# Kernel tuning notes

Measured on AMD Instinct MI355X. Metric: run time of the kernel, lower is better.

Reference implementation:

```python
import jax, jax.numpy as jnp
import numpy as np


def _causal_mask(n):
    # pixelSNAIL get_causal_mask: strict lower triangular (pixel i attends to pixels < i)
    return jnp.tril(jnp.ones((n, n), dtype=jnp.float32), k=-1)


def setup_inputs() -> dict:
    key = jax.random.key(0)
    kq, kk, kv = jax.random.split(key, 3)
    B, H, W, C, CM = 32, 32, 32, 128, 256
    return {
        "query": jax.random.normal(kq, (B, H, W, C), dtype=jnp.float32),
        "key": jax.random.normal(kk, (B, H, W, C), dtype=jnp.float32),
        "value": jax.random.normal(kv, (B, H, W, CM), dtype=jnp.float32),
    }


def reference(query, key, value):
    B = query.shape[0]
    C = key.shape[-1]
    CM = value.shape[-1]
    Nk = int(np.prod(key.shape[1:-1]))
    Nq = int(np.prod(query.shape[1:-1]))
    q = query.reshape(B, Nq, C)
    k = key.reshape(B, Nk, C)
    v = value.reshape(B, Nk, CM)
    # raw QK^T (no 1/sqrt(d) scaling in original)
    dot = jnp.einsum('bqc,bkc->bqk', q, k)
    # NON-STANDARD: softmax over full row first, then multiply by strict causal mask
    probs = jax.nn.softmax(dot, axis=-1) * _causal_mask(Nq)[None]
    mixed = jnp.einsum('bqk,bkm->bqm', probs, v)
    return mixed.reshape(query.shape[:-1] + (CM,))
```

## Files before the change

kernel.cpp:

```cpp
#include <hip/hip_runtime.h>


typedef __attribute__((ext_vector_type(8))) short short8;
typedef __attribute__((ext_vector_type(4))) float floatx4;

#define MFMA16(a, b, c) __builtin_amdgcn_mfma_f32_16x16x32_bf16((a), (b), (c), 0, 0, 0)

constexpr int N = 1024, C = 128, CM = 256, BATCH = 32;
constexpr int BM = 32;
constexpr int BN = 32;
constexpr int NT = N / BN;
constexpr int KFRAG = BN * C;
constexpr int VFRAG = BN * CM;
constexpr int PSTR = 40;

__device__ __forceinline__ unsigned short f2bf(float x) {
    unsigned int u = __float_as_uint(x);
    u += 0x7fffu + ((u >> 16) & 1u);
    return (unsigned short)(u >> 16);
}
__device__ __forceinline__ float bf2f(unsigned short h) {
    return __uint_as_float(((unsigned int)h) << 16);
}
__device__ __forceinline__ uint4 pack8(const unsigned short* s) {
    uint4 u;
    u.x = (unsigned)s[0] | ((unsigned)s[1] << 16);
    u.y = (unsigned)s[2] | ((unsigned)s[3] << 16);
    u.z = (unsigned)s[4] | ((unsigned)s[5] << 16);
    u.w = (unsigned)s[6] | ((unsigned)s[7] << 16);
    return u;
}
__device__ __forceinline__ void gl2lds16(const unsigned short* g, unsigned short* l) {
    __builtin_amdgcn_global_load_lds(
        (const __attribute__((address_space(1))) void*)g,
        (__attribute__((address_space(3))) void*)l, 16, 0, 0);
}

__global__ __launch_bounds__(256, 4)
void prep_kernel(const float* __restrict__ kg, const float* __restrict__ vg,
                 unsigned short* __restrict__ khi, unsigned short* __restrict__ klo,
                 unsigned short* __restrict__ vf)
{
    constexpr int KP = 132;
    constexpr int VP = 260;
    __shared__ __align__(16) float S[BN * VP];

    const int tid = threadIdx.x;
    const int tile = blockIdx.x, bat = blockIdx.y;
    const int n0 = tile * BN;
    const float* kb = kg + (size_t)bat * N * C;
    const float* vb = vg + (size_t)bat * N * CM;

#pragma unroll
    for (int i = 0; i < 4; ++i) {
        int f = tid + i * 256;
        int row = f >> 5, c4 = f & 31;
        float4 x = *(const float4*)(kb + (size_t)(n0 + row) * C + c4 * 4);
        *(float4*)(&S[row * KP + c4 * 4]) = x;
    }
    __syncthreads();
    {
        unsigned short* khb = khi + ((size_t)bat * NT + tile) * KFRAG;
        unsigned short* klb = klo + ((size_t)bat * NT + tile) * KFRAG;
#pragma unroll
        for (int i = 0; i < 2; ++i) {
            int ch = tid + i * 256;
            int r = ch & 15, qd = (ch >> 4) & 3, ks = (ch >> 6) & 3, t = ch >> 8;
            const float* src = &S[(t * 16 + r) * KP + ks * 32 + qd * 8];
            unsigned short hi[8], lo[8];
#pragma unroll
            for (int j = 0; j < 8; ++j) {
                float x = src[j];
                unsigned short h = f2bf(x);
                hi[j] = h;
                lo[j] = f2bf(x - bf2f(h));
            }
            *(uint4*)(khb + (size_t)ch * 8) = pack8(hi);
            *(uint4*)(klb + (size_t)ch * 8) = pack8(lo);
        }
    }
    __syncthreads();
#pragma unroll
    for (int i = 0; i < 8; ++i) {
        int f = tid + i * 256;
        int row = f >> 6, c4 = f & 63;
        float4 x = *(const float4*)(vb + (size_t)(n0 + row) * CM + c4 * 4);
        *(float4*)(&S[row * VP + c4 * 4]) = x;
    }
    __syncthreads();
    {
        unsigned short* vfb = vf + ((size_t)bat * NT + tile) * VFRAG;
#pragma unroll
        for (int i = 0; i < 4; ++i) {
            int ch = tid + i * 256;
            int r = ch & 15, qd = (ch >> 4) & 3, ct = ch >> 6;
            unsigned short o[8];
#pragma unroll
            for (int j = 0; j < 8; ++j)
                o[j] = f2bf(S[(qd * 8 + j) * VP + ct * 16 + r]);
            *(uint4*)(vfb + (size_t)ch * 8) = pack8(o);
        }
    }
}

__global__ __launch_bounds__(256, 4)
void attn_kernel(const float* __restrict__ qg, float* __restrict__ og,
                 const unsigned short* __restrict__ khi,
                 const unsigned short* __restrict__ klo,
                 const unsigned short* __restrict__ vf)
{
    __shared__ __align__(16) unsigned short sKhi[KFRAG];
    __shared__ __align__(16) unsigned short sKlo[KFRAG];
    __shared__ __align__(16) unsigned short sV[VFRAG];
    __shared__ __align__(16) unsigned short sP[4 * 16 * PSTR];

    const int tid = threadIdx.x;
    const int w = tid >> 6, ln = tid & 63;
    const int r = ln & 15, qd = ln >> 4;
    const int rowgrp = w >> 1;
    const int cmhalf = w & 1;
    const int bat = blockIdx.x;
    const int qt = blockIdx.y;
    const int q0 = qt * BM;

    const float* qb = qg + (size_t)bat * N * C;
    float* ob = og + (size_t)bat * N * CM;
    const unsigned short* khb = khi + (size_t)bat * NT * KFRAG;
    const unsigned short* klb = klo + (size_t)bat * NT * KFRAG;
    const unsigned short* vfb = vf + (size_t)bat * NT * VFRAG;

    short8 qhi[4], qlo[4];
    {
        const float* qr = qb + (size_t)(q0 + rowgrp * 16 + r) * C + qd * 8;
#pragma unroll
        for (int ks = 0; ks < 4; ++ks) {
            float4 a = *(const float4*)(qr + ks * 32);
            float4 b = *(const float4*)(qr + ks * 32 + 4);
            float xs[8] = {a.x, a.y, a.z, a.w, b.x, b.y, b.z, b.w};
            short8 h, l;
#pragma unroll
            for (int j = 0; j < 8; ++j) {
                unsigned short hb = f2bf(xs[j]);
                h[j] = (short)hb;
                l[j] = (short)f2bf(xs[j] - bf2f(hb));
            }
            qhi[ks] = h;
            qlo[ks] = l;
        }
    }

    floatx4 oacc[8];
#pragma unroll
    for (int ct = 0; ct < 8; ++ct) oacc[ct] = (floatx4){0.f, 0.f, 0.f, 0.f};
    float lsum[4] = {0.f, 0.f, 0.f, 0.f};
    const int irow = q0 + rowgrp * 16 + qd * 4;
    unsigned short* wP = &sP[w * 16 * PSTR];

    for (int tile = 0; tile < NT; ++tile) {
        const bool pv = (tile <= qt);

        {
            const unsigned short* sk = khb + (size_t)tile * KFRAG;
            gl2lds16(sk + (size_t)tid * 8,         &sKhi[tid * 8]);
            gl2lds16(sk + (size_t)(tid + 256) * 8, &sKhi[(tid + 256) * 8]);
            const unsigned short* sl = klb + (size_t)tile * KFRAG;
            gl2lds16(sl + (size_t)tid * 8,         &sKlo[tid * 8]);
            gl2lds16(sl + (size_t)(tid + 256) * 8, &sKlo[(tid + 256) * 8]);
            if (pv) {
                const unsigned short* sv = vfb + (size_t)tile * VFRAG;
#pragma unroll
                for (int i = 0; i < 4; ++i)
                    gl2lds16(sv + (size_t)(tid + i * 256) * 8, &sV[(tid + i * 256) * 8]);
            }
        }
        __syncthreads();

#pragma unroll
        for (int t = 0; t < 2; ++t) {
            floatx4 acc = (floatx4){0.f, 0.f, 0.f, 0.f};
#pragma unroll
            for (int ks = 0; ks < 4; ++ks) {
                short8 bh = *(const short8*)(&sKhi[(((t * 4 + ks) * 64) + ln) * 8]);
                short8 bl = *(const short8*)(&sKlo[(((t * 4 + ks) * 64) + ln) * 8]);
                acc = MFMA16(qhi[ks], bh, acc);
                acc = MFMA16(qlo[ks], bh, acc);
                acc = MFMA16(qhi[ks], bl, acc);
            }
            const int jglob = tile * BN + t * 16 + r;
#pragma unroll
            for (int rg = 0; rg < 4; ++rg) {
                float p = __expf(acc[rg] - 40.0f);
                lsum[rg] += p;
                if (pv) {
                    float pm = (jglob < irow + rg) ? p : 0.0f;
                    wP[(qd * 4 + rg) * PSTR + t * 16 + r] = f2bf(pm);
                }
            }
        }

        if (pv) {
            asm volatile("s_waitcnt lgkmcnt(0)" ::: "memory");
            short8 ap = *(const short8*)(&wP[r * PSTR + qd * 8]);
#pragma unroll
            for (int ct = 0; ct < 8; ++ct) {
                int ctg = cmhalf * 8 + ct;
                short8 bv = *(const short8*)(&sV[(ctg * 64 + ln) * 8]);
                oacc[ct] = MFMA16(ap, bv, oacc[ct]);
            }
        }
        __syncthreads();
    }

#pragma unroll
    for (int rg = 0; rg < 4; ++rg) {
        float v = lsum[rg];
        v += __shfl_xor(v, 1);
        v += __shfl_xor(v, 2);
        v += __shfl_xor(v, 4);
        v += __shfl_xor(v, 8);
        lsum[rg] = v;
    }

#pragma unroll
    for (int rg = 0; rg < 4; ++rg) {
        float inv = 1.0f / lsum[rg];
        float* orow = ob + (size_t)(q0 + rowgrp * 16 + qd * 4 + rg) * CM + cmhalf * 128;
#pragma unroll
        for (int ct = 0; ct < 8; ++ct)
            orow[ct * 16 + r] = oacc[ct][rg] * inv;
    }
}

extern "C" void kernel_launch(void* const* d_in, const int* in_sizes, int n_in,
                              void* d_out, int out_size, void* d_ws, size_t ws_size,
                              hipStream_t stream) {
    const float* q = (const float*)d_in[0];
    const float* k = (const float*)d_in[1];
    const float* v = (const float*)d_in[2];
    float* o = (float*)d_out;
    (void)n_in; (void)in_sizes; (void)out_size; (void)ws_size;

    unsigned short* khi = (unsigned short*)d_ws;
    unsigned short* klo = khi + (size_t)BATCH * NT * KFRAG;
    unsigned short* vf  = klo + (size_t)BATCH * NT * KFRAG;

    prep_kernel<<<dim3(NT, BATCH), dim3(256), 0, stream>>>(k, v, khi, klo, vf);
    attn_kernel<<<dim3(BATCH, N / BM), dim3(256), 0, stream>>>(q, o, khi, klo, vf);
}
```

Before: 175.0 us.

## Double-buffer K tiles, widen query tile to 64 rows, drop LDS staging in prep

The attention kernel now handles 64 query rows per block, with each wave owning 16 rows across all 256 value columns. This halves the number of times each K/V tile is streamed per batch. K hi/lo tiles are double-buffered, with the next tile prefetched through global_load_lds under explicit vmcnt waits and raw s_barrier, and the three split-bf16 MFMAs now use independent accumulators to break the dependency chain. The prep kernel drops its shared-memory staging and reads global memory directly, which gives strided uncoalesced V reads. The changes cost more accumulator registers (occupancy hint lowered to 2) and fewer blocks in the grid.

```diff
diff --git a/kernel.cpp b/kernel.cpp
--- a/kernel.cpp
+++ b/kernel.cpp
@@ -7,7 +7,7 @@
 #define MFMA16(a, b, c) __builtin_amdgcn_mfma_f32_16x16x32_bf16((a), (b), (c), 0, 0, 0)
 
 constexpr int N = 1024, C = 128, CM = 256, BATCH = 32;
-constexpr int BM = 32;
+constexpr int BM = 64;
 constexpr int BN = 32;
 constexpr int NT = N / BN;
 constexpr int KFRAG = BN * C;
@@ -36,89 +36,65 @@
         (__attribute__((address_space(3))) void*)l, 16, 0, 0);
 }
 
-__global__ __launch_bounds__(256, 4)
+__global__ __launch_bounds__(256, 8)
 void prep_kernel(const float* __restrict__ kg, const float* __restrict__ vg,
                  unsigned short* __restrict__ khi, unsigned short* __restrict__ klo,
                  unsigned short* __restrict__ vf)
 {
-    constexpr int KP = 132;
-    constexpr int VP = 260;
-    __shared__ __align__(16) float S[BN * VP];
-
     const int tid = threadIdx.x;
     const int tile = blockIdx.x, bat = blockIdx.y;
     const int n0 = tile * BN;
     const float* kb = kg + (size_t)bat * N * C;
     const float* vb = vg + (size_t)bat * N * CM;
-
+    unsigned short* khb = khi + ((size_t)bat * NT + tile) * KFRAG;
+    unsigned short* klb = klo + ((size_t)bat * NT + tile) * KFRAG;
+    unsigned short* vfb = vf + ((size_t)bat * NT + tile) * VFRAG;
+
+#pragma unroll
+    for (int i = 0; i < 2; ++i) {
+        int ch = tid + i * 256;
+        int r = ch & 15, qd = (ch >> 4) & 3, ks = (ch >> 6) & 3, t = ch >> 8;
+        const float* src = kb + (size_t)(n0 + t * 16 + r) * C + ks * 32 + qd * 8;
+        float4 a = *(const float4*)src;
+        float4 b = *(const float4*)(src + 4);
+        float xs[8] = {a.x, a.y, a.z, a.w, b.x, b.y, b.z, b.w};
+        unsigned short hi[8], lo[8];
+#pragma unroll
+        for (int j = 0; j < 8; ++j) {
+            unsigned short h = f2bf(xs[j]);
+            hi[j] = h;
+            lo[j] = f2bf(xs[j] - bf2f(h));
+        }
+        *(uint4*)(khb + (size_t)ch * 8) = pack8(hi);
+        *(uint4*)(klb + (size_t)ch * 8) = pack8(lo);
+    }
 #pragma unroll
     for (int i = 0; i < 4; ++i) {
-        int f = tid + i * 256;
-        int row = f >> 5, c4 = f & 31;
-        float4 x = *(const float4*)(kb + (size_t)(n0 + row) * C + c4 * 4);
-        *(float4*)(&S[row * KP + c4 * 4]) = x;
-    }
-    __syncthreads();
-    {
-        unsigned short* khb = khi + ((size_t)bat * NT + tile) * KFRAG;
-        unsigned short* klb = klo + ((size_t)bat * NT + tile) * KFRAG;
-#pragma unroll
-        for (int i = 0; i < 2; ++i) {
-            int ch = tid + i * 256;
-            int r = ch & 15, qd = (ch >> 4) & 3, ks = (ch >> 6) & 3, t = ch >> 8;
-            const float* src = &S[(t * 16 + r) * KP + ks * 32 + qd * 8];
-            unsigned short hi[8], lo[8];
-#pragma unroll
-            for (int j = 0; j < 8; ++j) {
-                float x = src[j];
-                unsigned short h = f2bf(x);
-                hi[j] = h;
-                lo[j] = f2bf(x - bf2f(h));
-            }
-            *(uint4*)(khb + (size_t)ch * 8) = pack8(hi);
-            *(uint4*)(klb + (size_t)ch * 8) = pack8(lo);
-        }
-    }
-    __syncthreads();
-#pragma unroll
-    for (int i = 0; i < 8; ++i) {
-        int f = tid + i * 256;
-        int row = f >> 6, c4 = f & 63;
-        float4 x = *(const float4*)(vb + (size_t)(n0 + row) * CM + c4 * 4);
-        *(float4*)(&S[row * VP + c4 * 4]) = x;
-    }
-    __syncthreads();
-    {
-        unsigned short* vfb = vf + ((size_t)bat * NT + tile) * VFRAG;
-#pragma unroll
-        for (int i = 0; i < 4; ++i) {
-            int ch = tid + i * 256;
-            int r = ch & 15, qd = (ch >> 4) & 3, ct = ch >> 6;
-            unsigned short o[8];
-#pragma unroll
-            for (int j = 0; j < 8; ++j)
-                o[j] = f2bf(S[(qd * 8 + j) * VP + ct * 16 + r]);
-            *(uint4*)(vfb + (size_t)ch * 8) = pack8(o);
-        }
-    }
-}
-
-__global__ __launch_bounds__(256, 4)
+        int ch = tid + i * 256;
+        int r = ch & 15, qd = (ch >> 4) & 3, ct = ch >> 6;
+        const float* src = vb + (size_t)(n0 + qd * 8) * CM + ct * 16 + r;
+        unsigned short o[8];
+#pragma unroll
+        for (int j = 0; j < 8; ++j)
+            o[j] = f2bf(src[(size_t)j * CM]);
+        *(uint4*)(vfb + (size_t)ch * 8) = pack8(o);
+    }
+}
+
+__global__ __launch_bounds__(256, 2)
 void attn_kernel(const float* __restrict__ qg, float* __restrict__ og,
                  const unsigned short* __restrict__ khi,
                  const unsigned short* __restrict__ klo,
                  const unsigned short* __restrict__ vf)
 {
-    __shared__ __align__(16) unsigned short sKhi[KFRAG];
-    __shared__ __align__(16) unsigned short sKlo[KFRAG];
+    __shared__ __align__(16) unsigned short sKhi[2][KFRAG];
+    __shared__ __align__(16) unsigned short sKlo[2][KFRAG];
     __shared__ __align__(16) unsigned short sV[VFRAG];
     __shared__ __align__(16) unsigned short sP[4 * 16 * PSTR];
 
     const int tid = threadIdx.x;
     const int w = tid >> 6, ln = tid & 63;
     const int r = ln & 15, qd = ln >> 4;
-    const int rowgrp = w >> 1;
-    const int cmhalf = w & 1;
     const int bat = blockIdx.x;
     const int qt = blockIdx.y;
     const int q0 = qt * BM;
@@ -131,7 +107,7 @@
 
     short8 qhi[4], qlo[4];
     {
-        const float* qr = qb + (size_t)(q0 + rowgrp * 16 + r) * C + qd * 8;
+        const float* qr = qb + (size_t)(q0 + w * 16 + r) * C + qd * 8;
 #pragma unroll
         for (int ks = 0; ks < 4; ++ks) {
             float4 a = *(const float4*)(qr + ks * 32);
@@ -149,66 +125,79 @@
         }
     }
 
-    floatx4 oacc[8];
-#pragma unroll
-    for (int ct = 0; ct < 8; ++ct) oacc[ct] = (floatx4){0.f, 0.f, 0.f, 0.f};
+    floatx4 oacc[16];
+#pragma unroll
+    for (int ct = 0; ct < 16; ++ct) oacc[ct] = (floatx4){0.f, 0.f, 0.f, 0.f};
     float lsum[4] = {0.f, 0.f, 0.f, 0.f};
-    const int irow = q0 + rowgrp * 16 + qd * 4;
+    const int irow = q0 + w * 16 + qd * 4;
     unsigned short* wP = &sP[w * 16 * PSTR];
 
+    gl2lds16(khb + (size_t)tid * 8,         &sKhi[0][tid * 8]);
+    gl2lds16(khb + (size_t)(tid + 256) * 8, &sKhi[0][(tid + 256) * 8]);
+    gl2lds16(klb + (size_t)tid * 8,         &sKlo[0][tid * 8]);
+    gl2lds16(klb + (size_t)(tid + 256) * 8, &sKlo[0][(tid + 256) * 8]);
+
     for (int tile = 0; tile < NT; ++tile) {
-        const bool pv = (tile <= qt);
-
-        {
-            const unsigned short* sk = khb + (size_t)tile * KFRAG;
-            gl2lds16(sk + (size_t)tid * 8,         &sKhi[tid * 8]);
-            gl2lds16(sk + (size_t)(tid + 256) * 8, &sKhi[(tid + 256) * 8]);
-            const unsigned short* sl = klb + (size_t)tile * KFRAG;
-            gl2lds16(sl + (size_t)tid * 8,         &sKlo[tid * 8]);
-            gl2lds16(sl + (size_t)(tid + 256) * 8, &sKlo[(tid + 256) * 8]);
-            if (pv) {
-                const unsigned short* sv = vfb + (size_t)tile * VFRAG;
-#pragma unroll
-                for (int i = 0; i < 4; ++i)
-                    gl2lds16(sv + (size_t)(tid + i * 256) * 8, &sV[(tid + i * 256) * 8]);
-            }
-        }
-        __syncthreads();
+        const bool pvt = (tile <= 2 * qt + 1);
+        const int cb = tile & 1;
+
+        if (pvt) {
+            const unsigned short* vs = vfb + (size_t)tile * VFRAG;
+#pragma unroll
+            for (int i = 0; i < 4; ++i)
+                gl2lds16(vs + (size_t)(tid + i * 256) * 8, &sV[(tid + i * 256) * 8]);
+        }
+        if (tile + 1 < NT) {
+            const unsigned short* k1 = khb + (size_t)(tile + 1) * KFRAG;
+            const unsigned short* l1 = klb + (size_t)(tile + 1) * KFRAG;
+            unsigned short* dh = &sKhi[cb ^ 1][0];
+            unsigned short* dl = &sKlo[cb ^ 1][0];
+            gl2lds16(k1 + (size_t)tid * 8,         dh + tid * 8);
+            gl2lds16(k1 + (size_t)(tid + 256) * 8, dh + (tid + 256) * 8);
+            gl2lds16(l1 + (size_t)tid * 8,         dl + tid * 8);
+            gl2lds16(l1 + (size_t)(tid + 256) * 8, dl + (tid + 256) * 8);
+            asm volatile("s_waitcnt vmcnt(4)" ::: "memory");
+        } else {
+            asm volatile("s_waitcnt vmcnt(0)" ::: "memory");
+        }
+        asm volatile("s_barrier" ::: "memory");
 
 #pragma unroll
         for (int t = 0; t < 2; ++t) {
-            floatx4 acc = (floatx4){0.f, 0.f, 0.f, 0.f};
+            floatx4 a0 = (floatx4){0.f, 0.f, 0.f, 0.f};
+            floatx4 a1 = (floatx4){0.f, 0.f, 0.f, 0.f};
+            floatx4 a2 = (floatx4){0.f, 0.f, 0.f, 0.f};
 #pragma unroll
             for (int ks = 0; ks < 4; ++ks) {
-                short8 bh = *(const short8*)(&sKhi[(((t * 4 + ks) * 64) + ln) * 8]);
-                short8 bl = *(const short8*)(&sKlo[(((t * 4 + ks) * 64) + ln) * 8]);
-                acc = MFMA16(qhi[ks], bh, acc);
-                acc = MFMA16(qlo[ks], bh, acc);
-                acc = MFMA16(qhi[ks], bl, acc);
+                short8 bh = *(const short8*)(&sKhi[cb][(((t * 4 + ks) * 64) + ln) * 8]);
+                short8 bl = *(const short8*)(&sKlo[cb][(((t * 4 + ks) * 64) + ln) * 8]);
+                a0 = MFMA16(qhi[ks], bh, a0);
+                a1 = MFMA16(qlo[ks], bh, a1);
+                a2 = MFMA16(qhi[ks], bl, a2);
             }
             const int jglob = tile * BN + t * 16 + r;
 #pragma unroll
             for (int rg = 0; rg < 4; ++rg) {
-                float p = __expf(acc[rg] - 40.0f);
+                float s = a0[rg] + a1[rg] + a2[rg];
+                float p = __expf(s - 40.0f);
                 lsum[rg] += p;
-                if (pv) {
+                if (pvt) {
                     float pm = (jglob < irow + rg) ? p : 0.0f;
                     wP[(qd * 4 + rg) * PSTR + t * 16 + r] = f2bf(pm);
                 }
             }
         }
 
-        if (pv) {
+        if (pvt) {
             asm volatile("s_waitcnt lgkmcnt(0)" ::: "memory");
             short8 ap = *(const short8*)(&wP[r * PSTR + qd * 8]);
 #pragma unroll
-            for (int ct = 0; ct < 8; ++ct) {
-                int ctg = cmhalf * 8 + ct;
-                short8 bv = *(const short8*)(&sV[(ctg * 64 + ln) * 8]);
+            for (int ct = 0; ct < 16; ++ct) {
+                short8 bv = *(const short8*)(&sV[(ct * 64 + ln) * 8]);
                 oacc[ct] = MFMA16(ap, bv, oacc[ct]);
             }
         }
-        __syncthreads();
+        asm volatile("s_barrier" ::: "memory");
     }
 
 #pragma unroll
@@ -224,9 +213,9 @@
 #pragma unroll
     for (int rg = 0; rg < 4; ++rg) {
         float inv = 1.0f / lsum[rg];
-        float* orow = ob + (size_t)(q0 + rowgrp * 16 + qd * 4 + rg) * CM + cmhalf * 128;
-#pragma unroll
-        for (int ct = 0; ct < 8; ++ct)
+        float* orow = ob + (size_t)(q0 + w * 16 + qd * 4 + rg) * CM;
+#pragma unroll
+        for (int ct = 0; ct < 16; ++ct)
             orow[ct * 16 + r] = oacc[ct][rg] * inv;
     }
 }
```

New measurement: 159.8 us. -8.7%, faster.
